# Optimization experiments

Measured on AMD Instinct MI355X. Metric: run time of the kernel, lower is better.

The kernel has to match this reference:

```python
import jax, jax.numpy as jnp
import numpy as np

# Module config (mirrors TritonMoEConfig)
N_EMBD = 768
EXPERT_SIZES = [(8, 512), (8, 1024)]  # (count, width) pairs
TOP_K = 8
NORM_TOPK_PROB = True

EXPERT_WIDTHS = []
for cnt, w in EXPERT_SIZES:
    EXPERT_WIDTHS += [w] * cnt
EXPERT_OFFSETS = np.concatenate([[0], np.cumsum(EXPERT_WIDTHS)]).astype(np.int64)
NUM_EXPERTS = len(EXPERT_WIDTHS)          # 16
TOTAL_WIDTH = int(EXPERT_OFFSETS[-1])     # 12288


def setup_inputs() -> dict:
    key = jax.random.key(0)
    k1, k2, k3, k4 = jax.random.split(key, 4)
    x = jax.random.normal(k1, (1, 2048, N_EMBD), dtype=jnp.float32)
    # trunc_normal(std=0.02) approximated by clipped normal
    router_w = jax.random.normal(k2, (NUM_EXPERTS, N_EMBD), dtype=jnp.float32) * 0.02
    w1 = jnp.clip(jax.random.normal(k3, (N_EMBD, TOTAL_WIDTH), dtype=jnp.float32) * 0.02, -0.06, 0.06)
    w2 = jnp.clip(jax.random.normal(k4, (TOTAL_WIDTH, N_EMBD), dtype=jnp.float32) * 0.02, -0.06, 0.06)
    return {"x": x, "router_w": router_w, "w1": w1, "w2": w2}


def reference(x, router_w, w1, w2):
    B, S, D = x.shape
    xt = x.reshape(-1, D)                              # [T, D]
    T = xt.shape[0]
    # 1. Route tokens: softmax over experts, top-k selection
    logits = jnp.einsum('td,ed->te', xt, router_w)     # [T, E]
    probs = jax.nn.softmax(logits, axis=-1)
    topk_w, topk_idx = jax.lax.top_k(probs, TOP_K)     # [T, K]
    if NORM_TOPK_PROB:
        topk_w = topk_w / jnp.sum(topk_w, axis=-1, keepdims=True)
    # Per-token combine weight for every expert (0 if not selected): [T, E]
    comb = jnp.zeros((T, NUM_EXPERTS), dtype=xt.dtype)
    comb = comb.at[jnp.arange(T)[:, None], topk_idx].add(topk_w)
    # 2-6. Grouped GEMM up (with activation) + down, combine with routing weights.
    # Experts have distinct widths, so loop over the fixed expert list.
    out = jnp.zeros_like(xt)
    for e in range(NUM_EXPERTS):
        off = int(EXPERT_OFFSETS[e])
        wd = EXPERT_WIDTHS[e]
        h = jax.nn.gelu(xt @ w1[:, off:off + wd])      # [T, wd]
        out = out + comb[:, e:e + 1] * (h @ w2[off:off + wd, :])
    return out.reshape(B, S, D)
```

## Files before the change

kernel.cpp:

```cpp
#include <hip/hip_runtime.h>
#include <hip/hip_bf16.h>


#define T_TOK 2048
#define D_EMB 768
#define W_TOT 12288
#define N_EXP 16

typedef __attribute__((ext_vector_type(4))) float f32x4;
typedef __attribute__((ext_vector_type(8))) short bf16x8;

typedef __attribute__((address_space(1))) const unsigned int as1c_u32;
typedef __attribute__((address_space(3))) unsigned int as3_u32;

__device__ __forceinline__ void gload16(const void* g, void* l) {
  __builtin_amdgcn_global_load_lds((as1c_u32*)g, (as3_u32*)l, 16, 0, 0);
}

__device__ __forceinline__ unsigned short f2bf(float f) {
  __hip_bfloat16 h = __float2bfloat16(f);
  return *reinterpret_cast<unsigned short*>(&h);
}

__device__ __forceinline__ float gelu_f(float x) {
  float x3 = x * x * x;
  float a = 0.7978845608028654f * __builtin_fmaf(0.044715f, x3, x);
  a = fminf(fmaxf(a, -20.f), 20.f);
  float e = __expf(-2.0f * a);
  float t = (1.0f - e) / (1.0f + e);
  return 0.5f * x * (1.0f + t);
}

__global__ __launch_bounds__(256) void transpose_cvt_kernel(
    const float* __restrict__ in, unsigned short* __restrict__ out, int R, int C) {
  __shared__ float tile[32][33];
  int c0 = blockIdx.x * 32;
  int r0 = blockIdx.y * 32;
  int i = threadIdx.x;
  {
    int r = i >> 3, c4 = (i & 7) * 4;
    float4 v = *(const float4*)(in + (size_t)(r0 + r) * C + c0 + c4);
    tile[r][c4 + 0] = v.x; tile[r][c4 + 1] = v.y;
    tile[r][c4 + 2] = v.z; tile[r][c4 + 3] = v.w;
  }
  __syncthreads();
  {
    int c = i >> 3, r4 = (i & 7) * 4;
    ushort4 o;
    o.x = f2bf(tile[r4 + 0][c]);
    o.y = f2bf(tile[r4 + 1][c]);
    o.z = f2bf(tile[r4 + 2][c]);
    o.w = f2bf(tile[r4 + 3][c]);
    *(ushort4*)(out + (size_t)(c0 + c) * R + r0 + r4) = o;
  }
}


__global__ __launch_bounds__(256) void router_kernel(
    const float* __restrict__ x, const float* __restrict__ rw,
    float* __restrict__ comb, unsigned short* __restrict__ xbout) {
  int tid = threadIdx.x, lane = tid & 63, w = tid >> 6;
  int t = blockIdx.x * 4 + w;
  const float* xr = x + (size_t)t * D_EMB;
  float xv[12];
#pragma unroll
  for (int i = 0; i < 12; ++i) xv[i] = xr[lane + 64 * i];
#pragma unroll
  for (int i = 0; i < 12; ++i)
    xbout[(size_t)t * D_EMB + lane + 64 * i] = f2bf(xv[i]);
  float lg[16];
#pragma unroll
  for (int e = 0; e < 16; ++e) {
    const float* we = rw + (size_t)e * D_EMB;
    float p = 0.f;
#pragma unroll
    for (int i = 0; i < 12; ++i) p = __builtin_fmaf(xv[i], we[lane + 64 * i], p);
#pragma unroll
    for (int off = 32; off >= 1; off >>= 1) p += __shfl_xor(p, off, 64);
    lg[e] = p;
  }
  float mx = lg[0];
#pragma unroll
  for (int e = 1; e < 16; ++e) mx = fmaxf(mx, lg[e]);
  float ex[16];
#pragma unroll
  for (int e = 0; e < 16; ++e) ex[e] = __expf(lg[e] - mx);
  float selsum = 0.f, myval = 0.f;
#pragma unroll
  for (int e = 0; e < 16; ++e) {
    int rank = 0;
#pragma unroll
    for (int e2 = 0; e2 < 16; ++e2)
      rank += (ex[e2] > ex[e]) || (ex[e2] == ex[e] && e2 < e);
    bool sel = rank < 8;
    float v = sel ? ex[e] : 0.f;
    selsum += v;
    if (e == lane) myval = v;
  }
  if (lane < 16) comb[(size_t)t * N_EXP + lane] = myval / selsum;
}


template <int EPI, int MAP, int LD>
__global__ __launch_bounds__(512, 4) void gemm_kernel(
    const unsigned short* __restrict__ Ag, const unsigned short* __restrict__ Bg,
    int ntiles, int kchunk, int splits,
    const float* __restrict__ comb, unsigned short* __restrict__ hout,
    float* __restrict__ pout) {
  __shared__ __align__(16) char smem[49152];

  const int tid = threadIdx.x;
  const int lane = tid & 63;
  const int wid = tid >> 6;
  const int wr = wid >> 2;
  const int wc = wid & 3;

  int mt, nt, zt;
  {
    int bid = blockIdx.x;
    if (MAP == 0) {
      int xcd = bid & 7, r = bid >> 3;
      nt = xcd * 12 + (r >> 3); mt = r & 7; zt = 0;
    } else {
      zt = bid % splits; int rr = bid / splits;
      nt = rr % 6; mt = rr / 6;
    }
  }
  const int rm0 = mt * 256;
  const int cn0 = nt * 128;
  const int kbeg = zt * kchunk;

  const int s = tid >> 2;
  const int scol = ((tid & 3) ^ (s & 3)) << 4;
  const int rA = (s & 63) + ((s >> 6) << 7);
  const char* pA0 = (const char*)Ag + ((size_t)(rm0 + rA) * LD + kbeg) * 2 + scol;
  const char* pA1 = pA0 + (size_t)64 * LD * 2;
  const char* pB  = (const char*)Bg + ((size_t)(cn0 + s) * LD + kbeg) * 2 + scol;

  const int slot = ((lane >> 4) ^ (lane & 3)) << 4;
  const int abase = wr * 4096 + (lane & 15) * 64 + slot;
  const int bbase = 32768 + (wc * 32 + (lane & 15)) * 64 + slot;

  f32x4 acc[8][2];
#pragma unroll
  for (int m = 0; m < 8; ++m)
#pragma unroll
    for (int n = 0; n < 2; ++n) acc[m][n] = (f32x4){0.f, 0.f, 0.f, 0.f};

  gload16(pB, smem + 32768 + wid * 1024);
  gload16(pA0, smem + wid * 1024);
  gload16(pA1, smem + 8192 + wid * 1024);
  pB += 64; pA0 += 64; pA1 += 64;
  __builtin_amdgcn_sched_barrier(0);

  int aoff = 0, boff = 0;
  bf16x8 a[4], b[2];
  for (int t = 0; t < ntiles; ++t) {
    const int nA = aoff ^ 16384;
    const int nB = boff ^ 8192;

    asm volatile("s_waitcnt vmcnt(1)" ::: "memory");
    __builtin_amdgcn_s_barrier();
    __builtin_amdgcn_sched_barrier(0);
#pragma unroll
    for (int m = 0; m < 4; ++m)
      a[m] = *(const bf16x8*)(smem + aoff + abase + m * 1024);
    b[0] = *(const bf16x8*)(smem + boff + bbase);
    b[1] = *(const bf16x8*)(smem + boff + bbase + 1024);
    gload16(pB, smem + 32768 + nB + wid * 1024);
    gload16(pA0, smem + nA + wid * 1024);
    __builtin_amdgcn_sched_barrier(0);
    __builtin_amdgcn_s_setprio(1);
#pragma unroll
    for (int m = 0; m < 4; ++m) {
      acc[m][0] = __builtin_amdgcn_mfma_f32_16x16x32_bf16(a[m], b[0], acc[m][0], 0, 0, 0);
      acc[m][1] = __builtin_amdgcn_mfma_f32_16x16x32_bf16(a[m], b[1], acc[m][1], 0, 0, 0);
    }
    __builtin_amdgcn_s_setprio(0);

    asm volatile("s_waitcnt vmcnt(2)" ::: "memory");
    __builtin_amdgcn_s_barrier();
    __builtin_amdgcn_sched_barrier(0);
#pragma unroll
    for (int m = 0; m < 4; ++m)
      a[m] = *(const bf16x8*)(smem + aoff + 8192 + abase + m * 1024);
    gload16(pA1, smem + nA + 8192 + wid * 1024);
    pB += 64; pA0 += 64; pA1 += 64;
    __builtin_amdgcn_sched_barrier(0);
    __builtin_amdgcn_s_setprio(1);
#pragma unroll
    for (int m = 0; m < 4; ++m) {
      acc[4 + m][0] = __builtin_amdgcn_mfma_f32_16x16x32_bf16(a[m], b[0], acc[4 + m][0], 0, 0, 0);
      acc[4 + m][1] = __builtin_amdgcn_mfma_f32_16x16x32_bf16(a[m], b[1], acc[4 + m][1], 0, 0, 0);
    }
    __builtin_amdgcn_s_setprio(0);

    aoff = nA; boff = nB;
  }

  asm volatile("s_waitcnt vmcnt(0)" ::: "memory");
  __syncthreads();

  const int r0 = (lane >> 4) * 4;
  const int cl = lane & 15;
  if constexpr (EPI == 1) {
    float* Cwf = (float*)smem;
    {
      int row = tid >> 1, c8 = (tid & 1) * 8;
      const float* sc = comb + (size_t)(rm0 + row) * N_EXP + c8;
      *(float4*)&Cwf[row * 16 + c8] = *(const float4*)sc;
      *(float4*)&Cwf[row * 16 + c8 + 4] = *(const float4*)(sc + 4);
    }
    __syncthreads();
#pragma unroll
    for (int n = 0; n < 2; ++n) {
      int colg = cn0 + wc * 32 + n * 16 + cl;
      int e = (colg < 4096) ? (colg >> 9) : (8 + ((colg - 4096) >> 10));
#pragma unroll
      for (int m = 0; m < 8; ++m) {
        int rl = wr * 128 + m * 16 + r0;
#pragma unroll
        for (int r = 0; r < 4; ++r) {
          float v = gelu_f(acc[m][n][r]) * Cwf[(rl + r) * 16 + e];
          hout[(size_t)(rm0 + rl + r) * W_TOT + colg] = f2bf(v);
        }
      }
    }
  } else {
    float* pz = pout + (size_t)zt * T_TOK * D_EMB;
#pragma unroll
    for (int n = 0; n < 2; ++n) {
      int colg = cn0 + wc * 32 + n * 16 + cl;
#pragma unroll
      for (int m = 0; m < 8; ++m) {
        int rl = wr * 128 + m * 16 + r0;
#pragma unroll
        for (int r = 0; r < 4; ++r)
          pz[(size_t)(rm0 + rl + r) * D_EMB + colg] = acc[m][n][r];
      }
    }
  }
}

__global__ __launch_bounds__(256) void reduce_kernel(
    const float* __restrict__ partial, float* __restrict__ out, int splits) {
  int i = (blockIdx.x * 256 + threadIdx.x) * 4;
  if (i >= T_TOK * D_EMB) return;
  float4 sv = *(const float4*)(partial + i);
  for (int sp = 1; sp < splits; ++sp) {
    float4 v = *(const float4*)(partial + (size_t)sp * T_TOK * D_EMB + i);
    sv.x += v.x; sv.y += v.y; sv.z += v.z; sv.w += v.w;
  }
  *(float4*)(out + i) = sv;
}


extern "C" void kernel_launch(void* const* d_in, const int* in_sizes, int n_in,
                              void* d_out, int out_size, void* d_ws, size_t ws_size,
                              hipStream_t stream) {
  const float* x = (const float*)d_in[0];
  const float* router_w = (const float*)d_in[1];
  const float* w1 = (const float*)d_in[2];
  const float* w2 = (const float*)d_in[3];
  float* out = (float*)d_out;

  char* ws = (char*)d_ws;
  size_t off = 0;
  auto alloc = [&](size_t bytes) {
    char* p = ws + off;
    off += (bytes + 255) & ~(size_t)255;
    return p;
  };
  unsigned short* xb  = (unsigned short*)alloc((size_t)T_TOK * D_EMB * 2);
  unsigned short* w1t = (unsigned short*)alloc((size_t)W_TOT * D_EMB * 2);
  unsigned short* w2t = (unsigned short*)alloc((size_t)D_EMB * W_TOT * 2);
  unsigned short* h   = (unsigned short*)alloc((size_t)T_TOK * W_TOT * 2);
  float* comb         = (float*)alloc((size_t)T_TOK * N_EXP * 4);

  int splits = 16;
  if (off + (size_t)16 * T_TOK * D_EMB * 4 > ws_size) splits = 8;
  if (off + (size_t)8 * T_TOK * D_EMB * 4 > ws_size) splits = 4;
  float* partial = (float*)alloc((size_t)splits * T_TOK * D_EMB * 4);
  int kchunk = W_TOT / splits;

  transpose_cvt_kernel<<<dim3(W_TOT / 32, D_EMB / 32), 256, 0, stream>>>(w1, w1t, D_EMB, W_TOT);
  transpose_cvt_kernel<<<dim3(D_EMB / 32, W_TOT / 32), 256, 0, stream>>>(w2, w2t, W_TOT, D_EMB);
  router_kernel<<<T_TOK / 4, 256, 0, stream>>>(x, router_w, comb, xb);

  gemm_kernel<1, 0, D_EMB><<<768, 512, 0, stream>>>(
      xb, w1t, D_EMB / 32, D_EMB, 1, comb, h, nullptr);

  gemm_kernel<0, 1, W_TOT><<<48 * splits, 512, 0, stream>>>(
      h, w2t, kchunk / 32, kchunk, splits, nullptr, nullptr, partial);

  reduce_kernel<<<(T_TOK * D_EMB) / 1024, 256, 0, stream>>>(partial, out, splits);
}
```

Measured before the change: 163.1 us.

## Enlarge GEMM tiles to 256x256 with triple-buffered LDS pipeline

The GEMM kernel moves from 256x128 to 256x256 output tiles per block, with 8x4 MFMA accumulators per wave. The K loop goes from double to triple buffering over 96KB of LDS, unrolled three tiles at a time. The down projection now uses a fixed split-K of 8 with 192 blocks, and the up projection uses 384 blocks. Larger tiles raise data reuse per LDS load and cut global traffic, but occupancy drops to 2 blocks per CU and there are fewer blocks than before, which may leave CUs idle on a 256-CU part.

```diff
diff --git a/kernel.cpp b/kernel.cpp
--- a/kernel.cpp
+++ b/kernel.cpp
@@ -101,13 +101,40 @@
 }
 
 
-template <int EPI, int MAP, int LD>
-__global__ __launch_bounds__(512, 4) void gemm_kernel(
+#define TILE(TT)                                                               \
+  {                                                                            \
+    asm volatile("s_waitcnt vmcnt(4)" ::: "memory");                           \
+    __builtin_amdgcn_s_barrier();                                              \
+    __builtin_amdgcn_sched_barrier(0);                                         \
+    _Pragma("unroll")                                                          \
+    for (int m = 0; m < 8; ++m)                                                \
+      a[m] = *(const bf16x8*)(smem + (TT) * 16384 + abase + m * 1024);         \
+    _Pragma("unroll")                                                          \
+    for (int n = 0; n < 4; ++n)                                                \
+      b[n] = *(const bf16x8*)(smem + 49152 + (TT) * 16384 + bbase + n * 1024); \
+    gload16(pA0, smem + (((TT) + 2) % 3) * 16384 + wid * 1024);                \
+    gload16(pA1, smem + (((TT) + 2) % 3) * 16384 + 8192 + wid * 1024);         \
+    gload16(pB0, smem + 49152 + (((TT) + 2) % 3) * 16384 + wid * 1024);        \
+    gload16(pB1, smem + 49152 + (((TT) + 2) % 3) * 16384 + 8192 + wid * 1024); \
+    pA0 += 64; pA1 += 64; pB0 += 64; pB1 += 64;                                \
+    __builtin_amdgcn_sched_barrier(0);                                         \
+    __builtin_amdgcn_s_setprio(1);                                             \
+    _Pragma("unroll")                                                          \
+    for (int m = 0; m < 8; ++m)                                                \
+      _Pragma("unroll")                                                        \
+      for (int n = 0; n < 4; ++n)                                              \
+        acc[m][n] = __builtin_amdgcn_mfma_f32_16x16x32_bf16(                   \
+            a[m], b[n], acc[m][n], 0, 0, 0);                                   \
+    __builtin_amdgcn_s_setprio(0);                                             \
+  }
+
+template <int EPI, int MAP>
+__global__ __launch_bounds__(512, 2) void gemm_kernel(
     const unsigned short* __restrict__ Ag, const unsigned short* __restrict__ Bg,
-    int ntiles, int kchunk, int splits,
+    int lda, int ldb, int ntiles, int kchunk,
     const float* __restrict__ comb, unsigned short* __restrict__ hout,
     float* __restrict__ pout) {
-  __shared__ __align__(16) char smem[49152];
+  __shared__ __align__(16) char smem[98304];
 
   const int tid = threadIdx.x;
   const int lane = tid & 63;
@@ -120,82 +147,50 @@
     int bid = blockIdx.x;
     if (MAP == 0) {
       int xcd = bid & 7, r = bid >> 3;
-      nt = xcd * 12 + (r >> 3); mt = r & 7; zt = 0;
+      nt = xcd * 6 + (r >> 3); mt = r & 7; zt = 0;
     } else {
-      zt = bid % splits; int rr = bid / splits;
-      nt = rr % 6; mt = rr / 6;
+      zt = bid & 7; int r = bid >> 3;
+      nt = r % 3; mt = r / 3;
     }
   }
   const int rm0 = mt * 256;
-  const int cn0 = nt * 128;
+  const int cn0 = nt * 256;
   const int kbeg = zt * kchunk;
 
-  const int s = tid >> 2;
-  const int scol = ((tid & 3) ^ (s & 3)) << 4;
-  const int rA = (s & 63) + ((s >> 6) << 7);
-  const char* pA0 = (const char*)Ag + ((size_t)(rm0 + rA) * LD + kbeg) * 2 + scol;
-  const char* pA1 = pA0 + (size_t)64 * LD * 2;
-  const char* pB  = (const char*)Bg + ((size_t)(cn0 + s) * LD + kbeg) * 2 + scol;
-
-  const int slot = ((lane >> 4) ^ (lane & 3)) << 4;
-  const int abase = wr * 4096 + (lane & 15) * 64 + slot;
-  const int bbase = 32768 + (wc * 32 + (lane & 15)) * 64 + slot;
-
-  f32x4 acc[8][2];
+  const int srow = tid >> 2;
+  const int scol = ((tid & 3) ^ (srow & 3)) << 4;
+  const char* pA0 = (const char*)Ag + ((size_t)(rm0 + srow) * lda + kbeg) * 2 + scol;
+  const char* pA1 = (const char*)Ag + ((size_t)(rm0 + 128 + srow) * lda + kbeg) * 2 + scol;
+  const char* pB0 = (const char*)Bg + ((size_t)(cn0 + srow) * ldb + kbeg) * 2 + scol;
+  const char* pB1 = (const char*)Bg + ((size_t)(cn0 + 128 + srow) * ldb + kbeg) * 2 + scol;
+
+  const int colsw = ((lane >> 4) ^ (lane & 3)) << 4;
+  const int abase = (wr * 128 + (lane & 15)) * 64 + colsw;
+  const int bbase = (wc * 64 + (lane & 15)) * 64 + colsw;
+
+  f32x4 acc[8][4];
 #pragma unroll
   for (int m = 0; m < 8; ++m)
 #pragma unroll
-    for (int n = 0; n < 2; ++n) acc[m][n] = (f32x4){0.f, 0.f, 0.f, 0.f};
-
-  gload16(pB, smem + 32768 + wid * 1024);
+    for (int n = 0; n < 4; ++n) acc[m][n] = (f32x4){0.f, 0.f, 0.f, 0.f};
+
   gload16(pA0, smem + wid * 1024);
   gload16(pA1, smem + 8192 + wid * 1024);
-  pB += 64; pA0 += 64; pA1 += 64;
+  gload16(pB0, smem + 49152 + wid * 1024);
+  gload16(pB1, smem + 49152 + 8192 + wid * 1024);
+  gload16(pA0 + 64, smem + 16384 + wid * 1024);
+  gload16(pA1 + 64, smem + 16384 + 8192 + wid * 1024);
+  gload16(pB0 + 64, smem + 49152 + 16384 + wid * 1024);
+  gload16(pB1 + 64, smem + 49152 + 16384 + 8192 + wid * 1024);
+  pA0 += 128; pA1 += 128; pB0 += 128; pB1 += 128;
   __builtin_amdgcn_sched_barrier(0);
 
-  int aoff = 0, boff = 0;
-  bf16x8 a[4], b[2];
-  for (int t = 0; t < ntiles; ++t) {
-    const int nA = aoff ^ 16384;
-    const int nB = boff ^ 8192;
-
-    asm volatile("s_waitcnt vmcnt(1)" ::: "memory");
-    __builtin_amdgcn_s_barrier();
-    __builtin_amdgcn_sched_barrier(0);
-#pragma unroll
-    for (int m = 0; m < 4; ++m)
-      a[m] = *(const bf16x8*)(smem + aoff + abase + m * 1024);
-    b[0] = *(const bf16x8*)(smem + boff + bbase);
-    b[1] = *(const bf16x8*)(smem + boff + bbase + 1024);
-    gload16(pB, smem + 32768 + nB + wid * 1024);
-    gload16(pA0, smem + nA + wid * 1024);
-    __builtin_amdgcn_sched_barrier(0);
-    __builtin_amdgcn_s_setprio(1);
-#pragma unroll
-    for (int m = 0; m < 4; ++m) {
-      acc[m][0] = __builtin_amdgcn_mfma_f32_16x16x32_bf16(a[m], b[0], acc[m][0], 0, 0, 0);
-      acc[m][1] = __builtin_amdgcn_mfma_f32_16x16x32_bf16(a[m], b[1], acc[m][1], 0, 0, 0);
-    }
-    __builtin_amdgcn_s_setprio(0);
-
-    asm volatile("s_waitcnt vmcnt(2)" ::: "memory");
-    __builtin_amdgcn_s_barrier();
-    __builtin_amdgcn_sched_barrier(0);
-#pragma unroll
-    for (int m = 0; m < 4; ++m)
-      a[m] = *(const bf16x8*)(smem + aoff + 8192 + abase + m * 1024);
-    gload16(pA1, smem + nA + 8192 + wid * 1024);
-    pB += 64; pA0 += 64; pA1 += 64;
-    __builtin_amdgcn_sched_barrier(0);
-    __builtin_amdgcn_s_setprio(1);
-#pragma unroll
-    for (int m = 0; m < 4; ++m) {
-      acc[4 + m][0] = __builtin_amdgcn_mfma_f32_16x16x32_bf16(a[m], b[0], acc[4 + m][0], 0, 0, 0);
-      acc[4 + m][1] = __builtin_amdgcn_mfma_f32_16x16x32_bf16(a[m], b[1], acc[4 + m][1], 0, 0, 0);
-    }
-    __builtin_amdgcn_s_setprio(0);
-
-    aoff = nA; boff = nB;
+  bf16x8 a[8], b[4];
+  const int nit = ntiles / 3;
+  for (int i = 0; i < nit; ++i) {
+    TILE(0)
+    TILE(1)
+    TILE(2)
   }
 
   asm volatile("s_waitcnt vmcnt(0)" ::: "memory");
@@ -207,14 +202,14 @@
     float* Cwf = (float*)smem;
     {
       int row = tid >> 1, c8 = (tid & 1) * 8;
-      const float* sc = comb + (size_t)(rm0 + row) * N_EXP + c8;
-      *(float4*)&Cwf[row * 16 + c8] = *(const float4*)sc;
-      *(float4*)&Cwf[row * 16 + c8 + 4] = *(const float4*)(sc + 4);
+      const float* s = comb + (size_t)(rm0 + row) * N_EXP + c8;
+      *(float4*)&Cwf[row * 16 + c8] = *(const float4*)s;
+      *(float4*)&Cwf[row * 16 + c8 + 4] = *(const float4*)(s + 4);
     }
     __syncthreads();
 #pragma unroll
-    for (int n = 0; n < 2; ++n) {
-      int colg = cn0 + wc * 32 + n * 16 + cl;
+    for (int n = 0; n < 4; ++n) {
+      int colg = cn0 + wc * 64 + n * 16 + cl;
       int e = (colg < 4096) ? (colg >> 9) : (8 + ((colg - 4096) >> 10));
 #pragma unroll
       for (int m = 0; m < 8; ++m) {
@@ -229,8 +224,8 @@
   } else {
     float* pz = pout + (size_t)zt * T_TOK * D_EMB;
 #pragma unroll
-    for (int n = 0; n < 2; ++n) {
-      int colg = cn0 + wc * 32 + n * 16 + cl;
+    for (int n = 0; n < 4; ++n) {
+      int colg = cn0 + wc * 64 + n * 16 + cl;
 #pragma unroll
       for (int m = 0; m < 8; ++m) {
         int rl = wr * 128 + m * 16 + r0;
@@ -246,12 +241,12 @@
     const float* __restrict__ partial, float* __restrict__ out, int splits) {
   int i = (blockIdx.x * 256 + threadIdx.x) * 4;
   if (i >= T_TOK * D_EMB) return;
-  float4 sv = *(const float4*)(partial + i);
+  float4 s = *(const float4*)(partial + i);
   for (int sp = 1; sp < splits; ++sp) {
     float4 v = *(const float4*)(partial + (size_t)sp * T_TOK * D_EMB + i);
-    sv.x += v.x; sv.y += v.y; sv.z += v.z; sv.w += v.w;
-  }
-  *(float4*)(out + i) = sv;
+    s.x += v.x; s.y += v.y; s.z += v.z; s.w += v.w;
+  }
+  *(float4*)(out + i) = s;
 }
 
 
@@ -277,9 +272,7 @@
   unsigned short* h   = (unsigned short*)alloc((size_t)T_TOK * W_TOT * 2);
   float* comb         = (float*)alloc((size_t)T_TOK * N_EXP * 4);
 
-  int splits = 16;
-  if (off + (size_t)16 * T_TOK * D_EMB * 4 > ws_size) splits = 8;
-  if (off + (size_t)8 * T_TOK * D_EMB * 4 > ws_size) splits = 4;
+  const int splits = 8;
   float* partial = (float*)alloc((size_t)splits * T_TOK * D_EMB * 4);
   int kchunk = W_TOT / splits;
 
@@ -287,11 +280,11 @@
   transpose_cvt_kernel<<<dim3(D_EMB / 32, W_TOT / 32), 256, 0, stream>>>(w2, w2t, W_TOT, D_EMB);
   router_kernel<<<T_TOK / 4, 256, 0, stream>>>(x, router_w, comb, xb);
 
-  gemm_kernel<1, 0, D_EMB><<<768, 512, 0, stream>>>(
-      xb, w1t, D_EMB / 32, D_EMB, 1, comb, h, nullptr);
-
-  gemm_kernel<0, 1, W_TOT><<<48 * splits, 512, 0, stream>>>(
-      h, w2t, kchunk / 32, kchunk, splits, nullptr, nullptr, partial);
+  gemm_kernel<1, 0><<<384, 512, 0, stream>>>(
+      xb, w1t, D_EMB, D_EMB, D_EMB / 32, D_EMB, comb, h, nullptr);
+
+  gemm_kernel<0, 1><<<192, 512, 0, stream>>>(
+      h, w2t, W_TOT, W_TOT, kchunk / 32, kchunk, nullptr, nullptr, partial);
 
   reduce_kernel<<<(T_TOK * D_EMB) / 1024, 256, 0, stream>>>(partial, out, splits);
 }
```

New measurement: 156.6 us. -4.0%, faster.
